# Optimization experiments

Measured on AMD Instinct MI355X. Metric: run time of the kernel, lower is better.

Reference implementation:

```python
import jax, jax.numpy as jnp
import numpy as np

A, NA, D_OBS, B = 16, 8, 64, 128  # agents, actions, obs dim, graphs
DZ = D_OBS + NA  # obs_z_input_dim = 72


def _mlp(x, W1, b1, W2, b2):
    # Linear -> leaky_relu(0.01) -> Linear, torch Linear convention (y = x @ W.T + b)
    return jax.nn.leaky_relu(x @ W1.T + b1) @ W2.T + b2


def setup_inputs() -> dict:
    key = jax.random.key(0)
    ks = iter(jax.random.split(key, 40))
    p = {}
    p["obs"] = jax.random.normal(next(ks), (B * A, D_OBS), jnp.float32)
    p["policies"] = jax.random.uniform(next(ks), (B * A, NA), jnp.float32)
    p["actions"] = jax.random.uniform(next(ks), (B * A, NA), jnp.float32)

    def mk(name, inp, out):
        p[name + "_w"] = jax.random.normal(next(ks), (out, inp), jnp.float32) / np.sqrt(inp).astype(np.float32)
        p[name + "_b"] = jax.random.normal(next(ks), (out,), jnp.float32) * 0.01

    mk("kw1", D_OBS, 64); mk("kw2", 64, 64)   # key_weight layers
    mk("qw1", D_OBS, 64); mk("qw2", 64, 64)   # query_weight layers
    mk("ko1", DZ, 64);    mk("ko2", 64, 64)   # key_obsz layers
    mk("qo1", DZ, 64);    mk("qo2", 64, 64)   # query_obsz layers
    mk("av1", DZ, 64);    mk("av2", 64, 64)   # attention_value_obsz layers
    mk("fv1", 128, 64);   mk("fv2", 64, 8)    # final_value layers
    return p


def reference(obs, policies, actions,
              kw1_w, kw1_b, kw2_w, kw2_b, qw1_w, qw1_b, qw2_w, qw2_b,
              ko1_w, ko1_b, ko2_w, ko2_b, qo1_w, qo1_b, qo2_w, qo2_b,
              av1_w, av1_b, av2_w, av2_b, fv1_w, fv1_b, fv2_w, fv2_b):
    d_k_w = jnp.sqrt(jnp.float32(kw2_w.shape[0]))
    d_k_o = jnp.sqrt(jnp.float32(ko2_w.shape[0]))
    Bn = obs.shape[0] // A
    obs_b = obs.reshape(Bn, A, -1)                      # [B,A,Dobs]
    pi = policies.reshape(Bn, A, NA)
    act = actions.reshape(Bn, A, NA)

    # --- DGL update_all on the fully-connected (with self-loop) per-batch graph ---
    key_z = _mlp(obs_b, kw1_w, kw1_b, kw2_w, kw2_b)     # [B,A,dk]
    query_z = _mlp(obs_b, qw1_w, qw1_b, qw2_w, qw2_b)
    score = jnp.einsum('bjd,bid->bij', key_z, query_z)  # src key j -> dst query i
    w = jax.nn.sigmoid(score / d_k_w)[..., None]        # [B,A,A,1], mailbox gate
    z = w * act[:, None] + (1.0 - w) * pi[:, None]      # [B,A(i),A(j),NA]
    weight_z = w.reshape(Bn * A, A, 1)

    # obs_z[b,i,j] = cat(obs[b,j], z[b,i,j])
    obs_rep = jnp.broadcast_to(obs_b[:, None], (Bn, A, A, obs_b.shape[-1]))
    obs_z = jnp.concatenate([obs_rep, z], axis=-1)      # [B,A,A,DZ]

    diag = jnp.arange(A)
    src = obs_z[:, diag, diag]                          # source_obs_z_: [B,A,DZ] (j==i entry)

    key_o = _mlp(src, ko1_w, ko1_b, ko2_w, ko2_b)       # broadcast over j
    query_o = _mlp(obs_z, qo1_w, qo1_b, qo2_w, qo2_b)   # [B,A,A,dk]
    score_o = jnp.einsum('bid,bijd->bij', key_o, query_o)
    weights_o = jax.nn.softmax(jnp.exp(jnp.clip(score_o / d_k_o, -5.0, 5.0)), axis=-1)  # [B,A,A]

    # obs_z_pi[b,i,j,k] = op[b,j] if k==j else obs_z[b,i,k], op = cat(obs, pi)
    op = jnp.concatenate([obs_b, pi], axis=-1)          # [B,A,DZ]
    m = jnp.eye(A, dtype=obs.dtype)[None, None, :, :, None]          # (j,k) mask
    obs_z_pi = obs_z[:, :, None] * (1.0 - m) + op[:, None, None] * m  # [B,A,A,A,DZ]

    attn_src = _mlp(src, av1_w, av1_b, av2_w, av2_b)                  # [B,A,O]
    attn_other = _mlp(obs_z_pi, av1_w, av1_b, av2_w, av2_b)           # [B,A,A,A,O]

    w_exp = weights_o[:, None, :, :, None]              # [b,i,j,k,1] = weights_o[b,j,k]
    mixed = jnp.mean(attn_other * w_exp, axis=-2)       # mean over k -> [B,A,A,O]
    src_rep = jnp.broadcast_to(attn_src[:, None], mixed.shape)
    node_features = jnp.concatenate([src_rep, mixed], axis=-1)        # [B,A,A,2O]
    value = _mlp(node_features, fv1_w, fv1_b, fv2_w, fv2_b)           # [B,A,A,8]

    weights_obsz = jnp.broadcast_to(w_exp, (Bn, A, A, A, 1))
    return value, weight_z, weights_obsz
```

## Files before the change

kernel.cpp:

```cpp
#include <hip/hip_runtime.h>

#define A_ 16
#define NA_ 8
#define DOBS_ 64

typedef _Float16 f16;
typedef f16 h2 __attribute__((ext_vector_type(2)));
typedef f16 v8h __attribute__((ext_vector_type(8)));
typedef float v4f __attribute__((ext_vector_type(4)));

__device__ __forceinline__ float fdot2f(h2 a, h2 b, float c) {
  return __builtin_amdgcn_fdot2(a, b, c, false);
}
__device__ __forceinline__ float lrelu(float x) { return x > 0.f ? x : 0.01f * x; }

struct P {
  const float *obs, *pol, *act;
  const float *kw1w, *kw1b, *kw2w, *kw2b, *qw1w, *qw1b, *qw2w, *qw2b;
  const float *ko1w, *ko1b, *ko2w, *ko2b, *qo1w, *qo1b, *qo2w, *qo2b;
  const float *av1w, *av1b, *av2w, *av2b, *fv1w, *fv1b, *fv2w, *fv2b;
  float *out0, *out1, *out2;
  float *wsig, *wo;
};


struct alignas(16) SM1 {
  f16 WAh[64 * 72], WAl[64 * 72];
  f16 obsh[16 * 72], obsl[16 * 72];
  f16 X1h[16 * 72], X1l[16 * 72];
  f16 X2h[16 * 72], X2l[16 * 72];
  float S2[16 * 68], S3[16 * 68];
  float G2[16 * 68];
  float wz[512];
  float bias8[8 * 64];
  float pi[128], act[128], wsig[256], wo[256], c0[16], e[256];
};

__device__ __forceinline__ v4f gemm_tile(const f16* Xh, const f16* Xl,
                                         const f16* Wh, const f16* Wl,
                                         float bv, int nt, int lane) {
  const int m = lane & 15, q = lane >> 4;
  v4f acc = {bv, bv, bv, bv};
  const v8h ah0 = *(const v8h*)(Xh + m * 72 + q * 8);
  const v8h ah1 = *(const v8h*)(Xh + m * 72 + 32 + q * 8);
  const v8h al0 = *(const v8h*)(Xl + m * 72 + q * 8);
  const v8h al1 = *(const v8h*)(Xl + m * 72 + 32 + q * 8);
  const f16* wr = Wh + (nt * 16 + m) * 72 + q * 8;
  const v8h bh0 = *(const v8h*)(wr);
  const v8h bh1 = *(const v8h*)(wr + 32);
  const f16* wr2 = Wl + (nt * 16 + m) * 72 + q * 8;
  const v8h bl0 = *(const v8h*)(wr2);
  const v8h bl1 = *(const v8h*)(wr2 + 32);
  acc = __builtin_amdgcn_mfma_f32_16x16x32_f16(ah0, bh0, acc, 0, 0, 0);
  acc = __builtin_amdgcn_mfma_f32_16x16x32_f16(ah1, bh1, acc, 0, 0, 0);
  acc = __builtin_amdgcn_mfma_f32_16x16x32_f16(ah0, bl0, acc, 0, 0, 0);
  acc = __builtin_amdgcn_mfma_f32_16x16x32_f16(ah1, bl1, acc, 0, 0, 0);
  acc = __builtin_amdgcn_mfma_f32_16x16x32_f16(al0, bh0, acc, 0, 0, 0);
  acc = __builtin_amdgcn_mfma_f32_16x16x32_f16(al1, bh1, acc, 0, 0, 0);
  return acc;
}

__device__ __forceinline__ void writeX(f16* Xh, f16* Xl, v4f acc, int nt, int lane, bool relu) {
  const int m = lane & 15, q = lane >> 4;
#pragma unroll
  for (int reg = 0; reg < 4; reg++) {
    float y = acc[reg];
    if (relu) y = lrelu(y);
    const f16 yh = (f16)y;
    Xh[(q * 4 + reg) * 72 + nt * 16 + m] = yh;
    Xl[(q * 4 + reg) * 72 + nt * 16 + m] = (f16)(y - (float)yh);
  }
}

__device__ __forceinline__ void putW(f16* Wh, f16* Wl, float4 v, int o, int r) {
  h2* dh = (h2*)(Wh + o * 72 + 4 * r);
  h2* dl = (h2*)(Wl + o * 72 + 4 * r);
  const f16 hx = (f16)v.x, hy = (f16)v.y, hz = (f16)v.z, hw = (f16)v.w;
  dh[0] = h2{hx, hy};
  dh[1] = h2{hz, hw};
  dl[0] = h2{(f16)(v.x - (float)hx), (f16)(v.y - (float)hy)};
  dl[1] = h2{(f16)(v.z - (float)hz), (f16)(v.w - (float)hw)};
}

__global__ __launch_bounds__(1024) void critic_k1(P p) {
  __shared__ SM1 s;
  const int tid = threadIdx.x;
  const int b = blockIdx.x;
  const int o = tid & 63, r = tid >> 6;
  const int w = r, lane = tid & 63, m = lane & 15, quad = lane >> 4;

  const float4 Rkw1 = *(const float4*)(p.kw1w + o * 64 + 4 * r);
  const float4 Rkw2 = *(const float4*)(p.kw2w + o * 64 + 4 * r);
  const float4 Rqw1 = *(const float4*)(p.qw1w + o * 64 + 4 * r);
  const float4 Rqw2 = *(const float4*)(p.qw2w + o * 64 + 4 * r);
  const float4 Rko2 = *(const float4*)(p.ko2w + o * 64 + 4 * r);
  const float4 Rko1 = *(const float4*)(p.ko1w + o * 72 + 4 * r);
  const float4 Rqo1 = *(const float4*)(p.qo1w + o * 72 + 4 * r);
  float4 Rqo2;
  Rqo2.x = p.qo2w[(4 * r + 0) * 64 + o];
  Rqo2.y = p.qo2w[(4 * r + 1) * 64 + o];
  Rqo2.z = p.qo2w[(4 * r + 2) * 64 + o];
  Rqo2.w = p.qo2w[(4 * r + 3) * 64 + o];
  const float Bqo2v = p.qo2b[o];
  float Rwzqo = 0.f;
  if (tid < 512) Rwzqo = p.qo1w[(tid >> 3) * 72 + 64 + (tid & 7)];

  if (tid < 512) {
    const float2 ov = ((const float2*)(p.obs + (size_t)b * 1024))[tid];
    const int e0 = 2 * tid, r0 = e0 >> 6, c0 = e0 & 63;
    const f16 hx = (f16)ov.x, hy = (f16)ov.y;
    *(h2*)(s.obsh + r0 * 72 + c0) = h2{hx, hy};
    *(h2*)(s.obsl + r0 * 72 + c0) = h2{(f16)(ov.x - (float)hx), (f16)(ov.y - (float)hy)};
  }
  if (tid < 128) s.pi[tid] = p.pol[(size_t)b * 128 + tid];
  else if (tid < 256) s.act[tid - 128] = p.act[(size_t)b * 128 + tid - 128];
  if (tid < 64) {
    s.bias8[tid] = p.kw1b[tid];        s.bias8[64 + tid] = p.kw2b[tid];
    s.bias8[128 + tid] = p.qw1b[tid];  s.bias8[192 + tid] = p.qw2b[tid];
    s.bias8[256 + tid] = p.ko1b[tid];  s.bias8[320 + tid] = p.ko2b[tid];
    s.bias8[384 + tid] = p.qo1b[tid];
  }
  if (tid < 512) s.wz[tid] = p.ko1w[(tid >> 3) * 72 + 64 + (tid & 7)];
  putW(s.WAh, s.WAl, Rkw1, o, r);
  __syncthreads();

  if (w < 4) {
    v4f a = gemm_tile(s.obsh, s.obsl, s.WAh, s.WAl, s.bias8[w * 16 + m], w, lane);
    writeX(s.X1h, s.X1l, a, w, lane, true);
  }
  __syncthreads();
  putW(s.WAh, s.WAl, Rkw2, o, r);
  __syncthreads();
  if (w < 4) {
    v4f a = gemm_tile(s.X1h, s.X1l, s.WAh, s.WAl, s.bias8[64 + w * 16 + m], w, lane);
#pragma unroll
    for (int reg = 0; reg < 4; reg++) s.S2[(quad * 4 + reg) * 68 + w * 16 + m] = a[reg];
  }
  __syncthreads();
  putW(s.WAh, s.WAl, Rqw1, o, r);
  __syncthreads();
  if (w < 4) {
    v4f a = gemm_tile(s.obsh, s.obsl, s.WAh, s.WAl, s.bias8[128 + w * 16 + m], w, lane);
    writeX(s.X2h, s.X2l, a, w, lane, true);
  }
  __syncthreads();
  putW(s.WAh, s.WAl, Rqw2, o, r);
  __syncthreads();
  if (w < 4) {
    v4f a = gemm_tile(s.X2h, s.X2l, s.WAh, s.WAl, s.bias8[192 + w * 16 + m], w, lane);
#pragma unroll
    for (int reg = 0; reg < 4; reg++) s.S3[(quad * 4 + reg) * 68 + w * 16 + m] = a[reg];
  }
  __syncthreads();

  {
    const int j = (tid >> 2) & 15, g = tid & 3;
    float a0 = 0.f, a1 = 0.f, a2 = 0.f, a3 = 0.f;
#pragma unroll
    for (int t4 = 0; t4 < 4; t4++) {
      const float4 qv = *(const float4*)(s.S3 + r * 68 + g * 16 + 4 * t4);
      const float4 kv = *(const float4*)(s.S2 + j * 68 + g * 16 + 4 * t4);
      a0 += qv.x * kv.x; a1 += qv.y * kv.y; a2 += qv.z * kv.z; a3 += qv.w * kv.w;
    }
    float sc = (a0 + a1) + (a2 + a3);
    sc += __shfl_xor(sc, 1);
    sc += __shfl_xor(sc, 2);
    if (g == 0) {
      const float wv = 1.f / (1.f + __expf(-sc * 0.125f));
      s.wsig[r * 16 + j] = wv;
      p.out1[(size_t)b * 256 + r * 16 + j] = wv;
      p.wsig[(size_t)b * 256 + r * 16 + j] = wv;
    }
    putW(s.WAh, s.WAl, Rko1, o, r);
  }
  __syncthreads();

  if (w < 4) {
    v4f a = gemm_tile(s.obsh, s.obsl, s.WAh, s.WAl, s.bias8[256 + w * 16 + m], w, lane);
    const int oo = w * 16 + m;
    float wzv[8];
    *(float4*)wzv = *(const float4*)(s.wz + oo * 8);
    *(float4*)(wzv + 4) = *(const float4*)(s.wz + oo * 8 + 4);
#pragma unroll
    for (int reg = 0; reg < 4; reg++) {
      const int rr = quad * 4 + reg;
      const float wrr = s.wsig[rr * 16 + rr];
      float zp = 0.f;
#pragma unroll
      for (int c = 0; c < 8; c++) {
        const float zc = s.pi[rr * 8 + c] + wrr * (s.act[rr * 8 + c] - s.pi[rr * 8 + c]);
        zp += wzv[c] * zc;
      }
      const float y = lrelu(a[reg] + zp);
      const f16 yh = (f16)y;
      s.X2h[rr * 72 + oo] = yh;
      s.X2l[rr * 72 + oo] = (f16)(y - (float)yh);
    }
  }
  __syncthreads();
  putW(s.WAh, s.WAl, Rko2, o, r);
  __syncthreads();
  if (w < 4) {
    v4f a = gemm_tile(s.X2h, s.X2l, s.WAh, s.WAl, s.bias8[320 + w * 16 + m], w, lane);
    writeX(s.X1h, s.X1l, a, w, lane, false);
  }
  __syncthreads();
  putW(s.WAh, s.WAl, Rqo2, o, r);
  __syncthreads();
  if (w < 4) {
    v4f a = gemm_tile(s.X1h, s.X1l, s.WAh, s.WAl, 0.f, w, lane);
#pragma unroll
    for (int reg = 0; reg < 4; reg++) s.S2[(quad * 4 + reg) * 68 + w * 16 + m] = a[reg];
  }
  {
    const float kv = (float)s.X1h[r * 72 + o] + (float)s.X1l[r * 72 + o];
    float t = kv * Bqo2v;
#pragma unroll
    for (int mm = 1; mm < 64; mm <<= 1) t += __shfl_xor(t, mm);
    if (o == 0) s.c0[r] = t;
  }
  __syncthreads();
  putW(s.WAh, s.WAl, Rqo1, o, r);
  if (tid < 512) {
    const int oo = tid >> 3, c = tid & 7;
    s.wz[(oo & 15) * 32 + (oo >> 4) * 8 + c] = Rwzqo;
  }
  __syncthreads();
  if (w < 4) {
    v4f a = gemm_tile(s.obsh, s.obsl, s.WAh, s.WAl, s.bias8[384 + w * 16 + m], w, lane);
#pragma unroll
    for (int reg = 0; reg < 4; reg++) s.G2[m * 68 + (quad * 4 + reg) * 4 + w] = a[reg];
  }
  __syncthreads();

  {
    const int j = (tid >> 2) & 15, g = tid & 3;
    const float wij = s.wsig[r * 16 + j];
    float z[8];
#pragma unroll
    for (int c = 0; c < 8; c++) z[c] = s.pi[j * 8 + c] + wij * (s.act[j * 8 + c] - s.pi[j * 8 + c]);
    float sc = 0.f;
#pragma unroll
    for (int t = 0; t < 16; t++) {
      const float4 wa = *(const float4*)(s.wz + t * 32 + g * 8);
      const float4 wb = *(const float4*)(s.wz + t * 32 + g * 8 + 4);
      float hv = s.G2[t * 68 + j * 4 + g]
        + wa.x * z[0] + wa.y * z[1] + wa.z * z[2] + wa.w * z[3]
        + wb.x * z[4] + wb.y * z[5] + wb.z * z[6] + wb.w * z[7];
      hv = lrelu(hv);
      sc += s.S2[r * 68 + g * 16 + t] * hv;
    }
    sc += __shfl_xor(sc, 1);
    sc += __shfl_xor(sc, 2);
    if (g == 0) {
      float yv = (sc + s.c0[r]) * 0.125f;
      yv = fminf(fmaxf(yv, -5.f), 5.f);
      s.e[r * 16 + j] = __expf(yv);
    }
  }
  __syncthreads();

  if (tid < 256) {
    const int i = tid >> 4, j = tid & 15;
    float mx = -1e30f;
#pragma unroll
    for (int jj = 0; jj < 16; jj++) mx = fmaxf(mx, s.e[i * 16 + jj]);
    float den = 0.f;
#pragma unroll
    for (int jj = 0; jj < 16; jj++) den += __expf(s.e[i * 16 + jj] - mx);
    const float val = __expf(s.e[i * 16 + j] - mx) / den;
    s.wo[i * 16 + j] = val;
    p.wo[(size_t)b * 256 + tid] = val;
  }
  __syncthreads();
  {
    const int q = tid >> 2, g = tid & 3, k = q & 15;
    *(float4*)(p.out2 + ((size_t)b * 256 + q) * 16 + 4 * g) =
        *(const float4*)(s.wo + k * 16 + 4 * g);
  }
}


struct alignas(16) SMem2 {
  f16 obsH[16][72];
  f16 AOsrcD[16 * 72];
  f16 APT[64 * 24];
  f16 AextH[16 * 40];
  f16 fv2pw[8 * 64];
  f16 slice[8][1536];
  union {
    struct { f16 av1H[64 * 96]; f16 av2H[64 * 72]; } av;
    f16 fv1H[64 * 136];
  } W;
  float pi[16][8], act[16][8], wsig[16][16];
  float av1b[64], av2b[64], fv1b[64], fv2b[8];
};

__device__ __forceinline__ v8h bfrag(const f16* Wm, int stride, int nt, int ks, int lane) {
  const int n = lane & 15, q = lane >> 4;
  return *(const v8h*)(Wm + (nt * 16 + n) * stride + ks * 32 + q * 8);
}

__device__ __forceinline__ void av_mlp(const SMem2& s, f16* Hbuf, v8h az, int lane, v4f acc2[4]) {
  const int m = lane & 15, q = lane >> 4;
  const v8h a0 = *(const v8h*)(&s.obsH[m][q * 8]);
  const v8h a1 = *(const v8h*)(&s.obsH[m][32 + q * 8]);
#pragma unroll
  for (int nt = 0; nt < 4; nt++) {
    const float bv = s.av1b[nt * 16 + m];
    v4f acc = {bv, bv, bv, bv};
    acc = __builtin_amdgcn_mfma_f32_16x16x32_f16(a0, bfrag(s.W.av.av1H, 96, nt, 0, lane), acc, 0, 0, 0);
    acc = __builtin_amdgcn_mfma_f32_16x16x32_f16(a1, bfrag(s.W.av.av1H, 96, nt, 1, lane), acc, 0, 0, 0);
    acc = __builtin_amdgcn_mfma_f32_16x16x32_f16(az, bfrag(s.W.av.av1H, 96, nt, 2, lane), acc, 0, 0, 0);
#pragma unroll
    for (int reg = 0; reg < 4; reg++)
      Hbuf[(q * 4 + reg) * 72 + nt * 16 + m] = (f16)lrelu(acc[reg]);
  }
  const v8h h0 = *(const v8h*)(Hbuf + m * 72 + q * 8);
  const v8h h1 = *(const v8h*)(Hbuf + m * 72 + 32 + q * 8);
#pragma unroll
  for (int nt = 0; nt < 4; nt++) {
    const float bv = s.av2b[nt * 16 + m];
    v4f acc = {bv, bv, bv, bv};
    acc = __builtin_amdgcn_mfma_f32_16x16x32_f16(h0, bfrag(s.W.av.av2H, 72, nt, 0, lane), acc, 0, 0, 0);
    acc = __builtin_amdgcn_mfma_f32_16x16x32_f16(h1, bfrag(s.W.av.av2H, 72, nt, 1, lane), acc, 0, 0, 0);
    acc2[nt] = acc;
  }
}

__global__ __launch_bounds__(512) void critic_k2(P p) {
  __shared__ SMem2 s;
  const int tid = threadIdx.x;
  const int b = blockIdx.x >> 1, ibase = (blockIdx.x & 1) * 8;
  const int w = tid >> 6, lane = tid & 63;
  const int m = lane & 15, quad = lane >> 4;
  const int i = ibase + w;

  float4 rfv[4];
#pragma unroll
  for (int qq = 0; qq < 4; qq++) rfv[qq] = ((const float4*)p.fv1w)[tid * 4 + qq];
  const float4 rav1a = ((const float4*)p.av1w)[tid * 2];
  const float4 rav1b = ((const float4*)p.av1w)[tid * 2 + 1];
  const float rav1c = p.av1w[4096 + tid];
  const float4 rav2a = ((const float4*)p.av2w)[tid * 2];
  const float4 rav2b = ((const float4*)p.av2w)[tid * 2 + 1];

  for (int k = tid; k < 1024; k += 512) s.obsH[k >> 6][k & 63] = (f16)p.obs[(size_t)b * 1024 + k];
  if (tid < 128) { s.pi[tid >> 3][tid & 7] = p.pol[(size_t)b * 128 + tid]; }
  else if (tid < 256) { int k = tid - 128; s.act[k >> 3][k & 7] = p.act[(size_t)b * 128 + k]; }
  for (int k = tid; k < 256; k += 512) s.wsig[k >> 4][k & 15] = p.wsig[(size_t)b * 256 + k];
  {
    const int kk = tid >> 5, j2 = tid & 31;
    float v = 0.f;
    if (j2 < 16) v = p.wo[(size_t)b * 256 + kk * 16 + j2] * 0.0625f;
    else if (j2 - 16 == kk) v = p.wo[(size_t)b * 256 + kk * 16 + kk] * 0.0625f;
    s.AextH[kk * 40 + j2] = (f16)v;
  }
  {
    float av1v[8] = {rav1a.x, rav1a.y, rav1a.z, rav1a.w, rav1b.x, rav1b.y, rav1b.z, rav1b.w};
#pragma unroll
    for (int e = 0; e < 8; e++) {
      const int k = tid * 8 + e, rr = k / 72, cc = k - rr * 72;
      s.W.av.av1H[rr * 96 + cc] = (f16)av1v[e];
    }
    const int k = 4096 + tid, rr = k / 72, cc = k - rr * 72;
    s.W.av.av1H[rr * 96 + cc] = (f16)rav1c;
  }
  {
    const int row = tid >> 3, c0 = 72 + (tid & 7) * 3;
#pragma unroll
    for (int c = 0; c < 3; c++) s.W.av.av1H[row * 96 + c0 + c] = (f16)0.f;
  }
  {
    float av2v[8] = {rav2a.x, rav2a.y, rav2a.z, rav2a.w, rav2b.x, rav2b.y, rav2b.z, rav2b.w};
#pragma unroll
    for (int e = 0; e < 8; e++) {
      const int k = tid * 8 + e;
      s.W.av.av2H[(k >> 6) * 72 + (k & 63)] = (f16)av2v[e];
    }
  }
  s.fv2pw[tid] = (f16)p.fv2w[tid];
  if (tid < 64) { s.av1b[tid] = p.av1b[tid]; s.av2b[tid] = p.av2b[tid]; s.fv1b[tid] = p.fv1b[tid]; }
  else if (tid < 72) s.fv2b[tid - 64] = p.fv2b[tid - 64];
  __syncthreads();

  f16* Sl = &s.slice[w][0];
  {
    v8h az = {};
    if (quad == 0) {
      const float wv = s.wsig[i][m];
#pragma unroll
      for (int c = 0; c < 8; c++) az[c] = (f16)(s.pi[m][c] + wv * (s.act[m][c] - s.pi[m][c]));
    }
    v4f acc2[4];
    av_mlp(s, Sl, az, lane, acc2);
#pragma unroll
    for (int nt = 0; nt < 4; nt++)
#pragma unroll
      for (int reg = 0; reg < 4; reg++)
        Sl[(nt * 16 + m) * 24 + quad * 4 + reg] = (f16)acc2[nt][reg];
  }
  if (w == 0) {
    v8h az = {};
    if (quad == 0) {
#pragma unroll
      for (int c = 0; c < 8; c++) az[c] = (f16)s.pi[m][c];
    }
    v4f acc2[4];
    av_mlp(s, s.APT, az, lane, acc2);
#pragma unroll
    for (int nt = 0; nt < 4; nt++)
#pragma unroll
      for (int reg = 0; reg < 4; reg++)
        s.APT[(nt * 16 + m) * 24 + quad * 4 + reg] = (f16)acc2[nt][reg];
  }
  if (w == 1) {
    v8h az = {};
    if (quad == 0) {
      const float wv = s.wsig[m][m];
#pragma unroll
      for (int c = 0; c < 8; c++) az[c] = (f16)(s.pi[m][c] + wv * (s.act[m][c] - s.pi[m][c]));
    }
    v4f acc2[4];
    av_mlp(s, s.AOsrcD, az, lane, acc2);
#pragma unroll
    for (int nt = 0; nt < 4; nt++)
#pragma unroll
      for (int reg = 0; reg < 4; reg++)
        s.AOsrcD[(quad * 4 + reg) * 72 + nt * 16 + m] = (f16)acc2[nt][reg];
  }
  __syncthreads();

#pragma unroll
  for (int qq = 0; qq < 4; qq++) {
    const int e0 = tid * 16 + qq * 4;
    h2* d = (h2*)&s.W.fv1H[(e0 >> 7) * 136 + (e0 & 127)];
    d[0] = h2{(f16)rfv[qq].x, (f16)rfv[qq].y};
    d[1] = h2{(f16)rfv[qq].z, (f16)rfv[qq].w};
  }
  __syncthreads();

  {
    const v8h am = *(const v8h*)(&s.AextH[m * 40 + quad * 8]);
    v4f macc[4];
#pragma unroll
    for (int nt = 0; nt < 4; nt++) {
      const int o = nt * 16 + m;
      v8h bf;
      if (quad < 2) {
        bf = *(const v8h*)(Sl + o * 24 + quad * 8);
      } else {
        const v8h apv = *(const v8h*)(&s.APT[o * 24 + (quad - 2) * 8]);
        const v8h aov = *(const v8h*)(Sl + o * 24 + (quad - 2) * 8);
        bf = apv - aov;
      }
      v4f z4 = {0.f, 0.f, 0.f, 0.f};
      macc[nt] = __builtin_amdgcn_mfma_f32_16x16x32_f16(am, bf, z4, 0, 0, 0);
    }
#pragma unroll
    for (int nt = 0; nt < 4; nt++)
#pragma unroll
      for (int reg = 0; reg < 4; reg++)
        Sl[(quad * 4 + reg) * 72 + nt * 16 + m] = (f16)macc[nt][reg];
  }

  {
    const v8h f0 = *(const v8h*)(&s.AOsrcD[m * 72 + quad * 8]);
    const v8h f1 = *(const v8h*)(&s.AOsrcD[m * 72 + 32 + quad * 8]);
    const v8h f2 = *(const v8h*)(Sl + m * 72 + quad * 8);
    const v8h f3 = *(const v8h*)(Sl + m * 72 + 32 + quad * 8);
#pragma unroll
    for (int nt = 0; nt < 4; nt++) {
      const float bv = s.fv1b[nt * 16 + m];
      v4f acc = {bv, bv, bv, bv};
      acc = __builtin_amdgcn_mfma_f32_16x16x32_f16(f0, bfrag(s.W.fv1H, 136, nt, 0, lane), acc, 0, 0, 0);
      acc = __builtin_amdgcn_mfma_f32_16x16x32_f16(f1, bfrag(s.W.fv1H, 136, nt, 1, lane), acc, 0, 0, 0);
      acc = __builtin_amdgcn_mfma_f32_16x16x32_f16(f2, bfrag(s.W.fv1H, 136, nt, 2, lane), acc, 0, 0, 0);
      acc = __builtin_amdgcn_mfma_f32_16x16x32_f16(f3, bfrag(s.W.fv1H, 136, nt, 3, lane), acc, 0, 0, 0);
#pragma unroll
      for (int reg = 0; reg < 4; reg++)
        Sl[(quad * 4 + reg) * 72 + nt * 16 + m] = (f16)lrelu(acc[reg]);
    }
  }
  {
    const int g2 = quad;
    float y0 = s.fv2b[2 * g2], y1 = s.fv2b[2 * g2 + 1];
#pragma unroll
    for (int o2 = 0; o2 < 32; o2++) {
      const h2 hh = *(const h2*)(Sl + m * 72 + 2 * o2);
      const h2 w0 = *(const h2*)(&s.fv2pw[(2 * g2) * 64 + 2 * o2]);
      const h2 w1 = *(const h2*)(&s.fv2pw[(2 * g2 + 1) * 64 + 2 * o2]);
      y0 = fdot2f(w0, hh, y0);
      y1 = fdot2f(w1, hh, y1);
    }
    *(float2*)(p.out0 + ((size_t)b * 256 + i * 16 + m) * 8 + 2 * g2) = make_float2(y0, y1);
  }
}

extern "C" void kernel_launch(void* const* d_in, const int* in_sizes, int n_in,
                              void* d_out, int out_size, void* d_ws, size_t ws_size,
                              hipStream_t stream) {
  P p;
  p.obs = (const float*)d_in[0];
  p.pol = (const float*)d_in[1];
  p.act = (const float*)d_in[2];
  p.kw1w = (const float*)d_in[3];  p.kw1b = (const float*)d_in[4];
  p.kw2w = (const float*)d_in[5];  p.kw2b = (const float*)d_in[6];
  p.qw1w = (const float*)d_in[7];  p.qw1b = (const float*)d_in[8];
  p.qw2w = (const float*)d_in[9];  p.qw2b = (const float*)d_in[10];
  p.ko1w = (const float*)d_in[11]; p.ko1b = (const float*)d_in[12];
  p.ko2w = (const float*)d_in[13]; p.ko2b = (const float*)d_in[14];
  p.qo1w = (const float*)d_in[15]; p.qo1b = (const float*)d_in[16];
  p.qo2w = (const float*)d_in[17]; p.qo2b = (const float*)d_in[18];
  p.av1w = (const float*)d_in[19]; p.av1b = (const float*)d_in[20];
  p.av2w = (const float*)d_in[21]; p.av2b = (const float*)d_in[22];
  p.fv1w = (const float*)d_in[23]; p.fv1b = (const float*)d_in[24];
  p.fv2w = (const float*)d_in[25]; p.fv2b = (const float*)d_in[26];

  const int Bn = in_sizes[0] / (A_ * DOBS_);
  p.out0 = (float*)d_out;
  p.out1 = p.out0 + (size_t)Bn * A_ * A_ * NA_;
  p.out2 = p.out1 + (size_t)Bn * A_ * A_;
  p.wsig = (float*)d_ws;
  p.wo = p.wsig + (size_t)Bn * 256;

  hipLaunchKernelGGL(critic_k1, dim3(Bn), dim3(1024), 0, stream, p);
  hipLaunchKernelGGL(critic_k2, dim3(2 * Bn), dim3(512), 0, stream, p);
}
```

Baseline: 130.4 us.

## Fuse both critic kernels into one launch with redundant per-graph front half

```diff
diff --git a/kernel.cpp b/kernel.cpp
--- a/kernel.cpp
+++ b/kernel.cpp
@@ -20,21 +20,49 @@
   const float *ko1w, *ko1b, *ko2w, *ko2b, *qo1w, *qo1b, *qo2w, *qo2b;
   const float *av1w, *av1b, *av2w, *av2b, *fv1w, *fv1b, *fv2w, *fv2b;
   float *out0, *out1, *out2;
-  float *wsig, *wo;
 };
 
-
-struct alignas(16) SM1 {
-  f16 WAh[64 * 72], WAl[64 * 72];
-  f16 obsh[16 * 72], obsl[16 * 72];
-  f16 X1h[16 * 72], X1l[16 * 72];
-  f16 X2h[16 * 72], X2l[16 * 72];
-  float S2[16 * 68], S3[16 * 68];
-  float G2[16 * 68];
-  float wz[512];
-  float bias8[8 * 64];
-  float pi[128], act[128], wsig[256], wo[256], c0[16], e[256];
+struct alignas(16) SM {
+  f16 obsh[16 * 72];
+  float pi[128];
+  float act[128];
+  float wsig[256];
+  float wo[256];
+  float c0[16];
+  f16 eh[256];
+  union {
+    struct {
+      f16 obsl[16 * 72];
+      f16 Wp1[64 * 72], Wp2[64 * 72];
+      f16 Wxh[64 * 72], Wxl[64 * 72];
+      f16 X1h[16 * 72], X1l[16 * 72];
+      f16 X2h[16 * 72], X2l[16 * 72];
+      float S2[16 * 68];
+      float S3G[16 * 68];
+      float wz[512];
+    } f;
+    struct {
+      f16 AOsrcD[16 * 72];
+      f16 APT[64 * 24];
+      f16 AextH[16 * 40];
+      f16 fv2pw[512];
+      f16 slice[8][1536];
+      union { struct { f16 av1H[64 * 96]; f16 av2H[64 * 72]; } av; f16 fv1H[64 * 136]; } W;
+      float av1b[64], av2b[64], fv1b[64], fv2b[8];
+    } bk;
+  } u;
 };
+
+__device__ __forceinline__ v4f gemm_plain(const f16* Xh, const f16* W, float bv, int nt, int lane) {
+  const int m = lane & 15, q = lane >> 4;
+  v4f acc = {bv, bv, bv, bv};
+  const v8h a0 = *(const v8h*)(Xh + m * 72 + q * 8);
+  const v8h a1 = *(const v8h*)(Xh + m * 72 + 32 + q * 8);
+  const f16* wr = W + (nt * 16 + m) * 72 + q * 8;
+  acc = __builtin_amdgcn_mfma_f32_16x16x32_f16(a0, *(const v8h*)wr, acc, 0, 0, 0);
+  acc = __builtin_amdgcn_mfma_f32_16x16x32_f16(a1, *(const v8h*)(wr + 32), acc, 0, 0, 0);
+  return acc;
+}
 
 __device__ __forceinline__ v4f gemm_tile(const f16* Xh, const f16* Xl,
                                          const f16* Wh, const f16* Wl,
@@ -72,9 +100,15 @@
   }
 }
 
-__device__ __forceinline__ void putW(f16* Wh, f16* Wl, float4 v, int o, int r) {
-  h2* dh = (h2*)(Wh + o * 72 + 4 * r);
-  h2* dl = (h2*)(Wl + o * 72 + 4 * r);
+__device__ __forceinline__ void putP(f16* W, float4 v, int o, int rq) {
+  h2* d = (h2*)(W + o * 72 + 4 * rq);
+  d[0] = h2{(f16)v.x, (f16)v.y};
+  d[1] = h2{(f16)v.z, (f16)v.w};
+}
+
+__device__ __forceinline__ void putW(f16* Wh, f16* Wl, float4 v, int o, int rq) {
+  h2* dh = (h2*)(Wh + o * 72 + 4 * rq);
+  h2* dl = (h2*)(Wl + o * 72 + 4 * rq);
   const f16 hx = (f16)v.x, hy = (f16)v.y, hz = (f16)v.z, hw = (f16)v.w;
   dh[0] = h2{hx, hy};
   dh[1] = h2{hz, hw};
@@ -82,105 +116,153 @@
   dl[1] = h2{(f16)(v.z - (float)hz), (f16)(v.w - (float)hw)};
 }
 
-__global__ __launch_bounds__(1024) void critic_k1(P p) {
-  __shared__ SM1 s;
+__device__ __forceinline__ v8h bfrag(const f16* Wm, int stride, int nt, int ks, int lane) {
+  const int n = lane & 15, q = lane >> 4;
+  return *(const v8h*)(Wm + (nt * 16 + n) * stride + ks * 32 + q * 8);
+}
+
+__device__ __forceinline__ void av_mlp2(const f16* obsh, const f16* av1H, const f16* av2H,
+                                        const float* av1b, const float* av2b,
+                                        f16* Hbuf, v8h az, int lane, v4f acc2[4]) {
+  const int m = lane & 15, q = lane >> 4;
+  const v8h a0 = *(const v8h*)(obsh + m * 72 + q * 8);
+  const v8h a1 = *(const v8h*)(obsh + m * 72 + 32 + q * 8);
+#pragma unroll
+  for (int nt = 0; nt < 4; nt++) {
+    const float bv = av1b[nt * 16 + m];
+    v4f acc = {bv, bv, bv, bv};
+    acc = __builtin_amdgcn_mfma_f32_16x16x32_f16(a0, bfrag(av1H, 96, nt, 0, lane), acc, 0, 0, 0);
+    acc = __builtin_amdgcn_mfma_f32_16x16x32_f16(a1, bfrag(av1H, 96, nt, 1, lane), acc, 0, 0, 0);
+    acc = __builtin_amdgcn_mfma_f32_16x16x32_f16(az, bfrag(av1H, 96, nt, 2, lane), acc, 0, 0, 0);
+#pragma unroll
+    for (int reg = 0; reg < 4; reg++)
+      Hbuf[(q * 4 + reg) * 72 + nt * 16 + m] = (f16)lrelu(acc[reg]);
+  }
+  const v8h h0 = *(const v8h*)(Hbuf + m * 72 + q * 8);
+  const v8h h1 = *(const v8h*)(Hbuf + m * 72 + 32 + q * 8);
+#pragma unroll
+  for (int nt = 0; nt < 4; nt++) {
+    const float bv = av2b[nt * 16 + m];
+    v4f acc = {bv, bv, bv, bv};
+    acc = __builtin_amdgcn_mfma_f32_16x16x32_f16(h0, bfrag(av2H, 72, nt, 0, lane), acc, 0, 0, 0);
+    acc = __builtin_amdgcn_mfma_f32_16x16x32_f16(h1, bfrag(av2H, 72, nt, 1, lane), acc, 0, 0, 0);
+    acc2[nt] = acc;
+  }
+}
+
+__global__ __launch_bounds__(512) void critic_fused(P p) {
+  __shared__ SM s;
   const int tid = threadIdx.x;
-  const int b = blockIdx.x;
-  const int o = tid & 63, r = tid >> 6;
-  const int w = r, lane = tid & 63, m = lane & 15, quad = lane >> 4;
-
-  const float4 Rkw1 = *(const float4*)(p.kw1w + o * 64 + 4 * r);
-  const float4 Rkw2 = *(const float4*)(p.kw2w + o * 64 + 4 * r);
-  const float4 Rqw1 = *(const float4*)(p.qw1w + o * 64 + 4 * r);
-  const float4 Rqw2 = *(const float4*)(p.qw2w + o * 64 + 4 * r);
-  const float4 Rko2 = *(const float4*)(p.ko2w + o * 64 + 4 * r);
-  const float4 Rko1 = *(const float4*)(p.ko1w + o * 72 + 4 * r);
-  const float4 Rqo1 = *(const float4*)(p.qo1w + o * 72 + 4 * r);
-  float4 Rqo2;
-  Rqo2.x = p.qo2w[(4 * r + 0) * 64 + o];
-  Rqo2.y = p.qo2w[(4 * r + 1) * 64 + o];
-  Rqo2.z = p.qo2w[(4 * r + 2) * 64 + o];
-  Rqo2.w = p.qo2w[(4 * r + 3) * 64 + o];
-  const float Bqo2v = p.qo2b[o];
-  float Rwzqo = 0.f;
-  if (tid < 512) Rwzqo = p.qo1w[(tid >> 3) * 72 + 64 + (tid & 7)];
-
-  if (tid < 512) {
+  const int b = blockIdx.x >> 1, ihalf = blockIdx.x & 1;
+  const int w = tid >> 6, lane = tid & 63;
+  const int m = lane & 15, quad = lane >> 4;
+  const int o = tid & 63, r8 = tid >> 6;
+
+  float4 Rkw1[2], Rkw2[2], Rqw1[2], Rqw2[2], Rko2[2], Rko1[2], Rqo1[2], Rqo2[2];
+#pragma unroll
+  for (int h = 0; h < 2; h++) {
+    const int rq = r8 + 8 * h;
+    Rkw1[h] = *(const float4*)(p.kw1w + o * 64 + 4 * rq);
+    Rkw2[h] = *(const float4*)(p.kw2w + o * 64 + 4 * rq);
+    Rqw1[h] = *(const float4*)(p.qw1w + o * 64 + 4 * rq);
+    Rqw2[h] = *(const float4*)(p.qw2w + o * 64 + 4 * rq);
+    Rko2[h] = *(const float4*)(p.ko2w + o * 64 + 4 * rq);
+    Rko1[h] = *(const float4*)(p.ko1w + o * 72 + 4 * rq);
+    Rqo1[h] = *(const float4*)(p.qo1w + o * 72 + 4 * rq);
+    Rqo2[h].x = p.qo2w[(4 * rq + 0) * 64 + o];
+    Rqo2[h].y = p.qo2w[(4 * rq + 1) * 64 + o];
+    Rqo2[h].z = p.qo2w[(4 * rq + 2) * 64 + o];
+    Rqo2[h].w = p.qo2w[(4 * rq + 3) * 64 + o];
+  }
+  const float Rwzko = p.ko1w[(tid >> 3) * 72 + 64 + (tid & 7)];
+  const float Rwzqo = p.qo1w[(tid >> 3) * 72 + 64 + (tid & 7)];
+  const int bi = (w & 3) * 16 + m;
+  const float bias1 = (w < 4 ? p.kw1b : p.qw1b)[bi];
+  const float bias2 = (w < 4 ? p.kw2b : p.qw2b)[bi];
+  const float bias3 = (w < 4 ? p.ko1b : p.qo1b)[bi];
+  const float bias4 = p.ko2b[bi];
+  const float Bqo2_0 = p.qo2b[tid & 31];
+  const float Bqo2_1 = p.qo2b[(tid & 31) + 32];
+  const float4 rav1a = ((const float4*)p.av1w)[tid * 2];
+  const float4 rav1b = ((const float4*)p.av1w)[tid * 2 + 1];
+  const float rav1c = p.av1w[4096 + tid];
+  const float4 rav2a = ((const float4*)p.av2w)[tid * 2];
+  const float4 rav2b = ((const float4*)p.av2w)[tid * 2 + 1];
+  float4 rfv[4];
+#pragma unroll
+  for (int qq = 0; qq < 4; qq++) rfv[qq] = ((const float4*)p.fv1w)[tid * 4 + qq];
+  const float rfv2 = p.fv2w[tid];
+  float rb1 = 0.f, rb2 = 0.f, rb3 = 0.f, rb4 = 0.f;
+  if (tid < 64) { rb1 = p.av1b[tid]; rb2 = p.av2b[tid]; rb3 = p.fv1b[tid]; }
+  if (tid < 8) rb4 = p.fv2b[tid];
+
+  {
     const float2 ov = ((const float2*)(p.obs + (size_t)b * 1024))[tid];
-    const int e0 = 2 * tid, r0 = e0 >> 6, c0 = e0 & 63;
+    const int e0 = 2 * tid, r0 = e0 >> 6, c0i = e0 & 63;
     const f16 hx = (f16)ov.x, hy = (f16)ov.y;
-    *(h2*)(s.obsh + r0 * 72 + c0) = h2{hx, hy};
-    *(h2*)(s.obsl + r0 * 72 + c0) = h2{(f16)(ov.x - (float)hx), (f16)(ov.y - (float)hy)};
+    *(h2*)(s.obsh + r0 * 72 + c0i) = h2{hx, hy};
+    *(h2*)(s.u.f.obsl + r0 * 72 + c0i) = h2{(f16)(ov.x - (float)hx), (f16)(ov.y - (float)hy)};
   }
   if (tid < 128) s.pi[tid] = p.pol[(size_t)b * 128 + tid];
   else if (tid < 256) s.act[tid - 128] = p.act[(size_t)b * 128 + tid - 128];
-  if (tid < 64) {
-    s.bias8[tid] = p.kw1b[tid];        s.bias8[64 + tid] = p.kw2b[tid];
-    s.bias8[128 + tid] = p.qw1b[tid];  s.bias8[192 + tid] = p.qw2b[tid];
-    s.bias8[256 + tid] = p.ko1b[tid];  s.bias8[320 + tid] = p.ko2b[tid];
-    s.bias8[384 + tid] = p.qo1b[tid];
-  }
-  if (tid < 512) s.wz[tid] = p.ko1w[(tid >> 3) * 72 + 64 + (tid & 7)];
-  putW(s.WAh, s.WAl, Rkw1, o, r);
-  __syncthreads();
-
-  if (w < 4) {
-    v4f a = gemm_tile(s.obsh, s.obsl, s.WAh, s.WAl, s.bias8[w * 16 + m], w, lane);
-    writeX(s.X1h, s.X1l, a, w, lane, true);
-  }
-  __syncthreads();
-  putW(s.WAh, s.WAl, Rkw2, o, r);
-  __syncthreads();
-  if (w < 4) {
-    v4f a = gemm_tile(s.X1h, s.X1l, s.WAh, s.WAl, s.bias8[64 + w * 16 + m], w, lane);
-#pragma unroll
-    for (int reg = 0; reg < 4; reg++) s.S2[(quad * 4 + reg) * 68 + w * 16 + m] = a[reg];
-  }
-  __syncthreads();
-  putW(s.WAh, s.WAl, Rqw1, o, r);
-  __syncthreads();
-  if (w < 4) {
-    v4f a = gemm_tile(s.obsh, s.obsl, s.WAh, s.WAl, s.bias8[128 + w * 16 + m], w, lane);
-    writeX(s.X2h, s.X2l, a, w, lane, true);
-  }
-  __syncthreads();
-  putW(s.WAh, s.WAl, Rqw2, o, r);
-  __syncthreads();
-  if (w < 4) {
-    v4f a = gemm_tile(s.X2h, s.X2l, s.WAh, s.WAl, s.bias8[192 + w * 16 + m], w, lane);
-#pragma unroll
-    for (int reg = 0; reg < 4; reg++) s.S3[(quad * 4 + reg) * 68 + w * 16 + m] = a[reg];
-  }
-  __syncthreads();
-
-  {
-    const int j = (tid >> 2) & 15, g = tid & 3;
+  s.u.f.wz[tid] = Rwzko;
+  putP(s.u.f.Wp1, Rkw1[0], o, r8); putP(s.u.f.Wp1, Rkw1[1], o, r8 + 8);
+  putP(s.u.f.Wp2, Rqw1[0], o, r8); putP(s.u.f.Wp2, Rqw1[1], o, r8 + 8);
+  putW(s.u.f.Wxh, s.u.f.Wxl, Rko1[0], o, r8); putW(s.u.f.Wxh, s.u.f.Wxl, Rko1[1], o, r8 + 8);
+  __syncthreads();
+
+  {
+    const f16* Wp = (w < 4) ? s.u.f.Wp1 : s.u.f.Wp2;
+    f16* Xo = (w < 4) ? s.u.f.X1h : s.u.f.X2h;
+    v4f a = gemm_plain(s.obsh, Wp, bias1, w & 3, lane);
+#pragma unroll
+    for (int reg = 0; reg < 4; reg++)
+      Xo[(quad * 4 + reg) * 72 + (w & 3) * 16 + m] = (f16)lrelu(a[reg]);
+  }
+  __syncthreads();
+  putP(s.u.f.Wp1, Rkw2[0], o, r8); putP(s.u.f.Wp1, Rkw2[1], o, r8 + 8);
+  putP(s.u.f.Wp2, Rqw2[0], o, r8); putP(s.u.f.Wp2, Rqw2[1], o, r8 + 8);
+  __syncthreads();
+
+  {
+    const f16* Wp = (w < 4) ? s.u.f.Wp1 : s.u.f.Wp2;
+    const f16* Xi = (w < 4) ? s.u.f.X1h : s.u.f.X2h;
+    float* So = (w < 4) ? s.u.f.S2 : s.u.f.S3G;
+    v4f a = gemm_plain(Xi, Wp, bias2, w & 3, lane);
+#pragma unroll
+    for (int reg = 0; reg < 4; reg++)
+      So[(quad * 4 + reg) * 68 + (w & 3) * 16 + m] = a[reg];
+  }
+  __syncthreads();
+
+  {
+    const int idx = tid >> 1, g2 = tid & 1;
+    const int i = idx >> 4, j = idx & 15;
     float a0 = 0.f, a1 = 0.f, a2 = 0.f, a3 = 0.f;
 #pragma unroll
-    for (int t4 = 0; t4 < 4; t4++) {
-      const float4 qv = *(const float4*)(s.S3 + r * 68 + g * 16 + 4 * t4);
-      const float4 kv = *(const float4*)(s.S2 + j * 68 + g * 16 + 4 * t4);
+    for (int t4 = 0; t4 < 8; t4++) {
+      const float4 qv = *(const float4*)(s.u.f.S3G + i * 68 + g2 * 32 + 4 * t4);
+      const float4 kv = *(const float4*)(s.u.f.S2 + j * 68 + g2 * 32 + 4 * t4);
       a0 += qv.x * kv.x; a1 += qv.y * kv.y; a2 += qv.z * kv.z; a3 += qv.w * kv.w;
     }
     float sc = (a0 + a1) + (a2 + a3);
     sc += __shfl_xor(sc, 1);
-    sc += __shfl_xor(sc, 2);
-    if (g == 0) {
+    if (g2 == 0) {
       const float wv = 1.f / (1.f + __expf(-sc * 0.125f));
-      s.wsig[r * 16 + j] = wv;
-      p.out1[(size_t)b * 256 + r * 16 + j] = wv;
-      p.wsig[(size_t)b * 256 + r * 16 + j] = wv;
-    }
-    putW(s.WAh, s.WAl, Rko1, o, r);
+      s.wsig[idx] = wv;
+      p.out1[(size_t)b * 256 + idx] = wv;
+    }
+    putW(s.u.f.Wp1, s.u.f.Wp2, Rqo1[0], o, r8);
+    putW(s.u.f.Wp1, s.u.f.Wp2, Rqo1[1], o, r8 + 8);
   }
   __syncthreads();
 
   if (w < 4) {
-    v4f a = gemm_tile(s.obsh, s.obsl, s.WAh, s.WAl, s.bias8[256 + w * 16 + m], w, lane);
+    v4f a = gemm_tile(s.obsh, s.u.f.obsl, s.u.f.Wxh, s.u.f.Wxl, bias3, w, lane);
     const int oo = w * 16 + m;
     float wzv[8];
-    *(float4*)wzv = *(const float4*)(s.wz + oo * 8);
-    *(float4*)(wzv + 4) = *(const float4*)(s.wz + oo * 8 + 4);
+    *(float4*)wzv = *(const float4*)(s.u.f.wz + oo * 8);
+    *(float4*)(wzv + 4) = *(const float4*)(s.u.f.wz + oo * 8 + 4);
 #pragma unroll
     for (int reg = 0; reg < 4; reg++) {
       const int rr = quad * 4 + reg;
@@ -193,207 +275,134 @@
       }
       const float y = lrelu(a[reg] + zp);
       const f16 yh = (f16)y;
-      s.X2h[rr * 72 + oo] = yh;
-      s.X2l[rr * 72 + oo] = (f16)(y - (float)yh);
-    }
-  }
-  __syncthreads();
-  putW(s.WAh, s.WAl, Rko2, o, r);
-  __syncthreads();
+      s.u.f.X2h[rr * 72 + oo] = yh;
+      s.u.f.X2l[rr * 72 + oo] = (f16)(y - (float)yh);
+    }
+  } else {
+    v4f a = gemm_tile(s.obsh, s.u.f.obsl, s.u.f.Wp1, s.u.f.Wp2, bias3, w - 4, lane);
+#pragma unroll
+    for (int reg = 0; reg < 4; reg++)
+      s.u.f.S3G[m * 68 + (quad * 4 + reg) * 4 + (w - 4)] = a[reg];
+  }
+  __syncthreads();
+
+  putW(s.u.f.Wxh, s.u.f.Wxl, Rko2[0], o, r8); putW(s.u.f.Wxh, s.u.f.Wxl, Rko2[1], o, r8 + 8);
+  putW(s.u.f.Wp1, s.u.f.Wp2, Rqo2[0], o, r8); putW(s.u.f.Wp1, s.u.f.Wp2, Rqo2[1], o, r8 + 8);
+  { const int oo = tid >> 3, c = tid & 7; s.u.f.wz[(oo & 15) * 32 + (oo >> 4) * 8 + c] = Rwzqo; }
+  __syncthreads();
+
   if (w < 4) {
-    v4f a = gemm_tile(s.X2h, s.X2l, s.WAh, s.WAl, s.bias8[320 + w * 16 + m], w, lane);
-    writeX(s.X1h, s.X1l, a, w, lane, false);
-  }
-  __syncthreads();
-  putW(s.WAh, s.WAl, Rqo2, o, r);
-  __syncthreads();
+    v4f a = gemm_tile(s.u.f.X2h, s.u.f.X2l, s.u.f.Wxh, s.u.f.Wxl, bias4, w, lane);
+    writeX(s.u.f.X1h, s.u.f.X1l, a, w, lane, false);
+  }
+  __syncthreads();
+
   if (w < 4) {
-    v4f a = gemm_tile(s.X1h, s.X1l, s.WAh, s.WAl, 0.f, w, lane);
-#pragma unroll
-    for (int reg = 0; reg < 4; reg++) s.S2[(quad * 4 + reg) * 68 + w * 16 + m] = a[reg];
-  }
-  {
-    const float kv = (float)s.X1h[r * 72 + o] + (float)s.X1l[r * 72 + o];
-    float t = kv * Bqo2v;
-#pragma unroll
-    for (int mm = 1; mm < 64; mm <<= 1) t += __shfl_xor(t, mm);
-    if (o == 0) s.c0[r] = t;
-  }
-  __syncthreads();
-  putW(s.WAh, s.WAl, Rqo1, o, r);
-  if (tid < 512) {
-    const int oo = tid >> 3, c = tid & 7;
-    s.wz[(oo & 15) * 32 + (oo >> 4) * 8 + c] = Rwzqo;
-  }
-  __syncthreads();
-  if (w < 4) {
-    v4f a = gemm_tile(s.obsh, s.obsl, s.WAh, s.WAl, s.bias8[384 + w * 16 + m], w, lane);
-#pragma unroll
-    for (int reg = 0; reg < 4; reg++) s.G2[m * 68 + (quad * 4 + reg) * 4 + w] = a[reg];
-  }
-  __syncthreads();
-
-  {
-    const int j = (tid >> 2) & 15, g = tid & 3;
-    const float wij = s.wsig[r * 16 + j];
+    v4f a = gemm_tile(s.u.f.X1h, s.u.f.X1l, s.u.f.Wp1, s.u.f.Wp2, 0.f, w, lane);
+#pragma unroll
+    for (int reg = 0; reg < 4; reg++)
+      s.u.f.S2[(quad * 4 + reg) * 68 + w * 16 + m] = a[reg];
+  }
+  {
+    const int rr = tid >> 5, cc = tid & 31;
+    const float kv0 = (float)s.u.f.X1h[rr * 72 + cc] + (float)s.u.f.X1l[rr * 72 + cc];
+    const float kv1 = (float)s.u.f.X1h[rr * 72 + cc + 32] + (float)s.u.f.X1l[rr * 72 + cc + 32];
+    float t = kv0 * Bqo2_0 + kv1 * Bqo2_1;
+#pragma unroll
+    for (int mk = 1; mk < 32; mk <<= 1) t += __shfl_xor(t, mk);
+    if (cc == 0) s.c0[rr] = t;
+  }
+  __syncthreads();
+
+  {
+    const int idx = tid >> 1, g2 = tid & 1;
+    const int i = idx >> 4, j = idx & 15;
+    const float wij = s.wsig[i * 16 + j];
     float z[8];
 #pragma unroll
     for (int c = 0; c < 8; c++) z[c] = s.pi[j * 8 + c] + wij * (s.act[j * 8 + c] - s.pi[j * 8 + c]);
     float sc = 0.f;
 #pragma unroll
-    for (int t = 0; t < 16; t++) {
-      const float4 wa = *(const float4*)(s.wz + t * 32 + g * 8);
-      const float4 wb = *(const float4*)(s.wz + t * 32 + g * 8 + 4);
-      float hv = s.G2[t * 68 + j * 4 + g]
-        + wa.x * z[0] + wa.y * z[1] + wa.z * z[2] + wa.w * z[3]
-        + wb.x * z[4] + wb.y * z[5] + wb.z * z[6] + wb.w * z[7];
-      hv = lrelu(hv);
-      sc += s.S2[r * 68 + g * 16 + t] * hv;
+    for (int gg = 2 * g2; gg <= 2 * g2 + 1; gg++) {
+#pragma unroll
+      for (int t = 0; t < 16; t++) {
+        const float4 wa = *(const float4*)(s.u.f.wz + t * 32 + gg * 8);
+        const float4 wb = *(const float4*)(s.u.f.wz + t * 32 + gg * 8 + 4);
+        float hv = s.u.f.S3G[t * 68 + j * 4 + gg]
+          + wa.x * z[0] + wa.y * z[1] + wa.z * z[2] + wa.w * z[3]
+          + wb.x * z[4] + wb.y * z[5] + wb.z * z[6] + wb.w * z[7];
+        hv = lrelu(hv);
+        sc += s.u.f.S2[i * 68 + gg * 16 + t] * hv;
+      }
     }
     sc += __shfl_xor(sc, 1);
-    sc += __shfl_xor(sc, 2);
-    if (g == 0) {
-      float yv = (sc + s.c0[r]) * 0.125f;
+    if (g2 == 0) {
+      float yv = (sc + s.c0[i]) * 0.125f;
       yv = fminf(fmaxf(yv, -5.f), 5.f);
-      s.e[r * 16 + j] = __expf(yv);
+      s.eh[idx] = (f16)__expf(yv);
     }
   }
   __syncthreads();
 
   if (tid < 256) {
     const int i = tid >> 4, j = tid & 15;
-    float mx = -1e30f;
-#pragma unroll
-    for (int jj = 0; jj < 16; jj++) mx = fmaxf(mx, s.e[i * 16 + jj]);
+    float ev[16]; float mx = -1e30f;
+#pragma unroll
+    for (int jj = 0; jj < 16; jj++) { ev[jj] = (float)s.eh[i * 16 + jj]; mx = fmaxf(mx, ev[jj]); }
     float den = 0.f;
 #pragma unroll
-    for (int jj = 0; jj < 16; jj++) den += __expf(s.e[i * 16 + jj] - mx);
-    const float val = __expf(s.e[i * 16 + j] - mx) / den;
-    s.wo[i * 16 + j] = val;
-    p.wo[(size_t)b * 256 + tid] = val;
-  }
-  __syncthreads();
-  {
-    const int q = tid >> 2, g = tid & 3, k = q & 15;
-    *(float4*)(p.out2 + ((size_t)b * 256 + q) * 16 + 4 * g) =
-        *(const float4*)(s.wo + k * 16 + 4 * g);
-  }
-}
-
-
-struct alignas(16) SMem2 {
-  f16 obsH[16][72];
-  f16 AOsrcD[16 * 72];
-  f16 APT[64 * 24];
-  f16 AextH[16 * 40];
-  f16 fv2pw[8 * 64];
-  f16 slice[8][1536];
-  union {
-    struct { f16 av1H[64 * 96]; f16 av2H[64 * 72]; } av;
-    f16 fv1H[64 * 136];
-  } W;
-  float pi[16][8], act[16][8], wsig[16][16];
-  float av1b[64], av2b[64], fv1b[64], fv2b[8];
-};
-
-__device__ __forceinline__ v8h bfrag(const f16* Wm, int stride, int nt, int ks, int lane) {
-  const int n = lane & 15, q = lane >> 4;
-  return *(const v8h*)(Wm + (nt * 16 + n) * stride + ks * 32 + q * 8);
-}
-
-__device__ __forceinline__ void av_mlp(const SMem2& s, f16* Hbuf, v8h az, int lane, v4f acc2[4]) {
-  const int m = lane & 15, q = lane >> 4;
-  const v8h a0 = *(const v8h*)(&s.obsH[m][q * 8]);
-  const v8h a1 = *(const v8h*)(&s.obsH[m][32 + q * 8]);
-#pragma unroll
-  for (int nt = 0; nt < 4; nt++) {
-    const float bv = s.av1b[nt * 16 + m];
-    v4f acc = {bv, bv, bv, bv};
-    acc = __builtin_amdgcn_mfma_f32_16x16x32_f16(a0, bfrag(s.W.av.av1H, 96, nt, 0, lane), acc, 0, 0, 0);
-    acc = __builtin_amdgcn_mfma_f32_16x16x32_f16(a1, bfrag(s.W.av.av1H, 96, nt, 1, lane), acc, 0, 0, 0);
-    acc = __builtin_amdgcn_mfma_f32_16x16x32_f16(az, bfrag(s.W.av.av1H, 96, nt, 2, lane), acc, 0, 0, 0);
-#pragma unroll
-    for (int reg = 0; reg < 4; reg++)
-      Hbuf[(q * 4 + reg) * 72 + nt * 16 + m] = (f16)lrelu(acc[reg]);
-  }
-  const v8h h0 = *(const v8h*)(Hbuf + m * 72 + q * 8);
-  const v8h h1 = *(const v8h*)(Hbuf + m * 72 + 32 + q * 8);
-#pragma unroll
-  for (int nt = 0; nt < 4; nt++) {
-    const float bv = s.av2b[nt * 16 + m];
-    v4f acc = {bv, bv, bv, bv};
-    acc = __builtin_amdgcn_mfma_f32_16x16x32_f16(h0, bfrag(s.W.av.av2H, 72, nt, 0, lane), acc, 0, 0, 0);
-    acc = __builtin_amdgcn_mfma_f32_16x16x32_f16(h1, bfrag(s.W.av.av2H, 72, nt, 1, lane), acc, 0, 0, 0);
-    acc2[nt] = acc;
-  }
-}
-
-__global__ __launch_bounds__(512) void critic_k2(P p) {
-  __shared__ SMem2 s;
-  const int tid = threadIdx.x;
-  const int b = blockIdx.x >> 1, ibase = (blockIdx.x & 1) * 8;
-  const int w = tid >> 6, lane = tid & 63;
-  const int m = lane & 15, quad = lane >> 4;
-  const int i = ibase + w;
-
-  float4 rfv[4];
-#pragma unroll
-  for (int qq = 0; qq < 4; qq++) rfv[qq] = ((const float4*)p.fv1w)[tid * 4 + qq];
-  const float4 rav1a = ((const float4*)p.av1w)[tid * 2];
-  const float4 rav1b = ((const float4*)p.av1w)[tid * 2 + 1];
-  const float rav1c = p.av1w[4096 + tid];
-  const float4 rav2a = ((const float4*)p.av2w)[tid * 2];
-  const float4 rav2b = ((const float4*)p.av2w)[tid * 2 + 1];
-
-  for (int k = tid; k < 1024; k += 512) s.obsH[k >> 6][k & 63] = (f16)p.obs[(size_t)b * 1024 + k];
-  if (tid < 128) { s.pi[tid >> 3][tid & 7] = p.pol[(size_t)b * 128 + tid]; }
-  else if (tid < 256) { int k = tid - 128; s.act[k >> 3][k & 7] = p.act[(size_t)b * 128 + k]; }
-  for (int k = tid; k < 256; k += 512) s.wsig[k >> 4][k & 15] = p.wsig[(size_t)b * 256 + k];
+    for (int jj = 0; jj < 16; jj++) den += __expf(ev[jj] - mx);
+    s.wo[tid] = __expf(ev[j] - mx) / den;
+  }
+  {
+    float av1v[8] = {rav1a.x, rav1a.y, rav1a.z, rav1a.w, rav1b.x, rav1b.y, rav1b.z, rav1b.w};
+#pragma unroll
+    for (int e = 0; e < 8; e++) {
+      const int k = tid * 8 + e, rr = k / 72, cc = k - rr * 72;
+      s.u.bk.W.av.av1H[rr * 96 + cc] = (f16)av1v[e];
+    }
+    const int k = 4096 + tid, rr = k / 72, cc = k - rr * 72;
+    s.u.bk.W.av.av1H[rr * 96 + cc] = (f16)rav1c;
+    const int row = tid >> 3, c0p = 72 + (tid & 7) * 3;
+#pragma unroll
+    for (int c = 0; c < 3; c++) s.u.bk.W.av.av1H[row * 96 + c0p + c] = (f16)0.f;
+    float av2v[8] = {rav2a.x, rav2a.y, rav2a.z, rav2a.w, rav2b.x, rav2b.y, rav2b.z, rav2b.w};
+#pragma unroll
+    for (int e = 0; e < 8; e++) {
+      const int k2 = tid * 8 + e;
+      s.u.bk.W.av.av2H[(k2 >> 6) * 72 + (k2 & 63)] = (f16)av2v[e];
+    }
+    s.u.bk.fv2pw[tid] = (f16)rfv2;
+    if (tid < 64) { s.u.bk.av1b[tid] = rb1; s.u.bk.av2b[tid] = rb2; s.u.bk.fv1b[tid] = rb3; }
+    if (tid < 8) s.u.bk.fv2b[tid] = rb4;
+  }
+  __syncthreads();
+
   {
     const int kk = tid >> 5, j2 = tid & 31;
     float v = 0.f;
-    if (j2 < 16) v = p.wo[(size_t)b * 256 + kk * 16 + j2] * 0.0625f;
-    else if (j2 - 16 == kk) v = p.wo[(size_t)b * 256 + kk * 16 + kk] * 0.0625f;
-    s.AextH[kk * 40 + j2] = (f16)v;
-  }
-  {
-    float av1v[8] = {rav1a.x, rav1a.y, rav1a.z, rav1a.w, rav1b.x, rav1b.y, rav1b.z, rav1b.w};
-#pragma unroll
-    for (int e = 0; e < 8; e++) {
-      const int k = tid * 8 + e, rr = k / 72, cc = k - rr * 72;
-      s.W.av.av1H[rr * 96 + cc] = (f16)av1v[e];
-    }
-    const int k = 4096 + tid, rr = k / 72, cc = k - rr * 72;
-    s.W.av.av1H[rr * 96 + cc] = (f16)rav1c;
-  }
-  {
-    const int row = tid >> 3, c0 = 72 + (tid & 7) * 3;
-#pragma unroll
-    for (int c = 0; c < 3; c++) s.W.av.av1H[row * 96 + c0 + c] = (f16)0.f;
-  }
-  {
-    float av2v[8] = {rav2a.x, rav2a.y, rav2a.z, rav2a.w, rav2b.x, rav2b.y, rav2b.z, rav2b.w};
-#pragma unroll
-    for (int e = 0; e < 8; e++) {
-      const int k = tid * 8 + e;
-      s.W.av.av2H[(k >> 6) * 72 + (k & 63)] = (f16)av2v[e];
-    }
-  }
-  s.fv2pw[tid] = (f16)p.fv2w[tid];
-  if (tid < 64) { s.av1b[tid] = p.av1b[tid]; s.av2b[tid] = p.av2b[tid]; s.fv1b[tid] = p.fv1b[tid]; }
-  else if (tid < 72) s.fv2b[tid - 64] = p.fv2b[tid - 64];
-  __syncthreads();
-
-  f16* Sl = &s.slice[w][0];
+    if (j2 < 16) v = s.wo[kk * 16 + j2] * 0.0625f;
+    else if (j2 - 16 == kk) v = s.wo[kk * 16 + kk] * 0.0625f;
+    s.u.bk.AextH[kk * 40 + j2] = (f16)v;
+    const int q_ = tid >> 1, g2_ = tid & 1, k_ = q_ & 15;
+    float* dst = p.out2 + ((size_t)b * 256 + q_) * 16 + 8 * g2_;
+    *(float4*)(dst) = *(const float4*)(s.wo + k_ * 16 + 8 * g2_);
+    *(float4*)(dst + 4) = *(const float4*)(s.wo + k_ * 16 + 8 * g2_ + 4);
+  }
+  __syncthreads();
+
+  const int i_ = ihalf * 8 + w;
+  f16* Sl = &s.u.bk.slice[w][0];
   {
     v8h az = {};
     if (quad == 0) {
-      const float wv = s.wsig[i][m];
-#pragma unroll
-      for (int c = 0; c < 8; c++) az[c] = (f16)(s.pi[m][c] + wv * (s.act[m][c] - s.pi[m][c]));
+      const float wv = s.wsig[i_ * 16 + m];
+#pragma unroll
+      for (int c = 0; c < 8; c++)
+        az[c] = (f16)(s.pi[m * 8 + c] + wv * (s.act[m * 8 + c] - s.pi[m * 8 + c]));
     }
     v4f acc2[4];
-    av_mlp(s, Sl, az, lane, acc2);
+    av_mlp2(s.obsh, s.u.bk.W.av.av1H, s.u.bk.W.av.av2H, s.u.bk.av1b, s.u.bk.av2b, Sl, az, lane, acc2);
 #pragma unroll
     for (int nt = 0; nt < 4; nt++)
 #pragma unroll
@@ -404,54 +413,55 @@
     v8h az = {};
     if (quad == 0) {
 #pragma unroll
-      for (int c = 0; c < 8; c++) az[c] = (f16)s.pi[m][c];
+      for (int c = 0; c < 8; c++) az[c] = (f16)s.pi[m * 8 + c];
     }
     v4f acc2[4];
-    av_mlp(s, s.APT, az, lane, acc2);
+    av_mlp2(s.obsh, s.u.bk.W.av.av1H, s.u.bk.W.av.av2H, s.u.bk.av1b, s.u.bk.av2b, s.u.bk.APT, az, lane, acc2);
 #pragma unroll
     for (int nt = 0; nt < 4; nt++)
 #pragma unroll
       for (int reg = 0; reg < 4; reg++)
-        s.APT[(nt * 16 + m) * 24 + quad * 4 + reg] = (f16)acc2[nt][reg];
+        s.u.bk.APT[(nt * 16 + m) * 24 + quad * 4 + reg] = (f16)acc2[nt][reg];
   }
   if (w == 1) {
     v8h az = {};
     if (quad == 0) {
-      const float wv = s.wsig[m][m];
-#pragma unroll
-      for (int c = 0; c < 8; c++) az[c] = (f16)(s.pi[m][c] + wv * (s.act[m][c] - s.pi[m][c]));
+      const float wv = s.wsig[m * 16 + m];
+#pragma unroll
+      for (int c = 0; c < 8; c++)
+        az[c] = (f16)(s.pi[m * 8 + c] + wv * (s.act[m * 8 + c] - s.pi[m * 8 + c]));
     }
     v4f acc2[4];
-    av_mlp(s, s.AOsrcD, az, lane, acc2);
+    av_mlp2(s.obsh, s.u.bk.W.av.av1H, s.u.bk.W.av.av2H, s.u.bk.av1b, s.u.bk.av2b, s.u.bk.AOsrcD, az, lane, acc2);
 #pragma unroll
     for (int nt = 0; nt < 4; nt++)
 #pragma unroll
       for (int reg = 0; reg < 4; reg++)
-        s.AOsrcD[(quad * 4 + reg) * 72 + nt * 16 + m] = (f16)acc2[nt][reg];
+        s.u.bk.AOsrcD[(quad * 4 + reg) * 72 + nt * 16 + m] = (f16)acc2[nt][reg];
   }
   __syncthreads();
 
 #pragma unroll
   for (int qq = 0; qq < 4; qq++) {
     const int e0 = tid * 16 + qq * 4;
-    h2* d = (h2*)&s.W.fv1H[(e0 >> 7) * 136 + (e0 & 127)];
+    h2* d = (h2*)&s.u.bk.W.fv1H[(e0 >> 7) * 136 + (e0 & 127)];
     d[0] = h2{(f16)rfv[qq].x, (f16)rfv[qq].y};
     d[1] = h2{(f16)rfv[qq].z, (f16)rfv[qq].w};
   }
   __syncthreads();
 
   {
-    const v8h am = *(const v8h*)(&s.AextH[m * 40 + quad * 8]);
+    const v8h am = *(const v8h*)(&s.u.bk.AextH[m * 40 + quad * 8]);
     v4f macc[4];
 #pragma unroll
     for (int nt = 0; nt < 4; nt++) {
-      const int o = nt * 16 + m;
+      const int oo = nt * 16 + m;
       v8h bf;
       if (quad < 2) {
-        bf = *(const v8h*)(Sl + o * 24 + quad * 8);
+        bf = *(const v8h*)(Sl + oo * 24 + quad * 8);
       } else {
-        const v8h apv = *(const v8h*)(&s.APT[o * 24 + (quad - 2) * 8]);
-        const v8h aov = *(const v8h*)(Sl + o * 24 + (quad - 2) * 8);
+        const v8h apv = *(const v8h*)(&s.u.bk.APT[oo * 24 + (quad - 2) * 8]);
+        const v8h aov = *(const v8h*)(Sl + oo * 24 + (quad - 2) * 8);
         bf = apv - aov;
       }
       v4f z4 = {0.f, 0.f, 0.f, 0.f};
@@ -463,20 +473,19 @@
       for (int reg = 0; reg < 4; reg++)
         Sl[(quad * 4 + reg) * 72 + nt * 16 + m] = (f16)macc[nt][reg];
   }
-
-  {
-    const v8h f0 = *(const v8h*)(&s.AOsrcD[m * 72 + quad * 8]);
-    const v8h f1 = *(const v8h*)(&s.AOsrcD[m * 72 + 32 + quad * 8]);
+  {
+    const v8h f0 = *(const v8h*)(&s.u.bk.AOsrcD[m * 72 + quad * 8]);
+    const v8h f1 = *(const v8h*)(&s.u.bk.AOsrcD[m * 72 + 32 + quad * 8]);
     const v8h f2 = *(const v8h*)(Sl + m * 72 + quad * 8);
     const v8h f3 = *(const v8h*)(Sl + m * 72 + 32 + quad * 8);
 #pragma unroll
     for (int nt = 0; nt < 4; nt++) {
-      const float bv = s.fv1b[nt * 16 + m];
+      const float bv = s.u.bk.fv1b[nt * 16 + m];
       v4f acc = {bv, bv, bv, bv};
-      acc = __builtin_amdgcn_mfma_f32_16x16x32_f16(f0, bfrag(s.W.fv1H, 136, nt, 0, lane), acc, 0, 0, 0);
-      acc = __builtin_amdgcn_mfma_f32_16x16x32_f16(f1, bfrag(s.W.fv1H, 136, nt, 1, lane), acc, 0, 0, 0);
-      acc = __builtin_amdgcn_mfma_f32_16x16x32_f16(f2, bfrag(s.W.fv1H, 136, nt, 2, lane), acc, 0, 0, 0);
-      acc = __builtin_amdgcn_mfma_f32_16x16x32_f16(f3, bfrag(s.W.fv1H, 136, nt, 3, lane), acc, 0, 0, 0);
+      acc = __builtin_amdgcn_mfma_f32_16x16x32_f16(f0, bfrag(s.u.bk.W.fv1H, 136, nt, 0, lane), acc, 0, 0, 0);
+      acc = __builtin_amdgcn_mfma_f32_16x16x32_f16(f1, bfrag(s.u.bk.W.fv1H, 136, nt, 1, lane), acc, 0, 0, 0);
+      acc = __builtin_amdgcn_mfma_f32_16x16x32_f16(f2, bfrag(s.u.bk.W.fv1H, 136, nt, 2, lane), acc, 0, 0, 0);
+      acc = __builtin_amdgcn_mfma_f32_16x16x32_f16(f3, bfrag(s.u.bk.W.fv1H, 136, nt, 3, lane), acc, 0, 0, 0);
 #pragma unroll
       for (int reg = 0; reg < 4; reg++)
         Sl[(quad * 4 + reg) * 72 + nt * 16 + m] = (f16)lrelu(acc[reg]);
@@ -484,16 +493,16 @@
   }
   {
     const int g2 = quad;
-    float y0 = s.fv2b[2 * g2], y1 = s.fv2b[2 * g2 + 1];
+    float y0 = s.u.bk.fv2b[2 * g2], y1 = s.u.bk.fv2b[2 * g2 + 1];
 #pragma unroll
     for (int o2 = 0; o2 < 32; o2++) {
       const h2 hh = *(const h2*)(Sl + m * 72 + 2 * o2);
-      const h2 w0 = *(const h2*)(&s.fv2pw[(2 * g2) * 64 + 2 * o2]);
-      const h2 w1 = *(const h2*)(&s.fv2pw[(2 * g2 + 1) * 64 + 2 * o2]);
+      const h2 w0 = *(const h2*)(&s.u.bk.fv2pw[(2 * g2) * 64 + 2 * o2]);
+      const h2 w1 = *(const h2*)(&s.u.bk.fv2pw[(2 * g2 + 1) * 64 + 2 * o2]);
       y0 = fdot2f(w0, hh, y0);
       y1 = fdot2f(w1, hh, y1);
     }
-    *(float2*)(p.out0 + ((size_t)b * 256 + i * 16 + m) * 8 + 2 * g2) = make_float2(y0, y1);
+    *(float2*)(p.out0 + ((size_t)b * 256 + i_ * 16 + m) * 8 + 2 * g2) = make_float2(y0, y1);
   }
 }
 
@@ -521,9 +530,6 @@
   p.out0 = (float*)d_out;
   p.out1 = p.out0 + (size_t)Bn * A_ * A_ * NA_;
   p.out2 = p.out1 + (size_t)Bn * A_ * A_;
-  p.wsig = (float*)d_ws;
-  p.wo = p.wsig + (size_t)Bn * 256;
-
-  hipLaunchKernelGGL(critic_k1, dim3(Bn), dim3(1024), 0, stream, p);
-  hipLaunchKernelGGL(critic_k2, dim3(2 * Bn), dim3(512), 0, stream, p);
-}
+
+  hipLaunchKernelGGL(critic_fused, dim3(2 * Bn), dim3(512), 0, stream, p);
+}
```

New measurement: 127.6 us. 1.02x faster.
